# Performance work log

Measured on AMD Instinct MI355X. Metric: run time of the kernel, lower is better.

## Reference

```python
import jax, jax.numpy as jnp
import numpy as np

CAPACITY = 1_000_000
IN_FEATURES = 64
OUT_FEATURES = 64


def setup_inputs() -> dict:
    key = jax.random.key(0)
    k1, k2, k3 = jax.random.split(key, 3)
    query = jax.random.normal(k1, (IN_FEATURES,), dtype=jnp.float32)
    keys = jax.random.normal(k2, (CAPACITY, IN_FEATURES), dtype=jnp.float32)
    values = jax.random.normal(k3, (CAPACITY, OUT_FEATURES), dtype=jnp.float32)
    return {"query": query, "keys": keys, "values": values}


def reference(query, keys, values):
    # attention: [capacity] = keys [C, Din] @ query [Din]
    scores = keys @ query
    attention = jax.nn.softmax(scores, axis=0)
    # out: [Dout] = attention [C] @ values [C, Dout]
    out = attention @ values
    # usage-tracking argmax (softmax is monotone, argmax of scores == argmax of attention)
    amax = jnp.argmax(scores)
    return out, amax
```

## Files before the change

kernel.cpp:

```cpp
#include <hip/hip_runtime.h>
#include <math.h>

#define C_CAP 1000000
#define DIM 64

#define SCORES_OFF 0
#define P1_OFF     1000000
#define HDR_OFF    1010000
#define ACC_OFF    1010064

#define NB1 1024
#define NW1 (NB1 * 4)
#define NTILES (C_CAP / 16)
#define NB3 2048
#define NW3 (NB3 * 4)
#define NCHUNKS (C_CAP / 64)

__global__ __launch_bounds__(256, 4) void nd_scores(
    const float* __restrict__ query,
    const float* __restrict__ keys,
    float* __restrict__ ws, int ntiles, int stride)
{
    const int tid  = threadIdx.x;
    const int lane = tid & 63;
    const int wave = tid >> 6;
    const int cl   = lane & 15;
    const int g    = lane >> 4;
    const int wglobal = blockIdx.x * 4 + wave;

    const float4 q4 = ((const float4*)query)[cl];
    const float4* __restrict__ k4p = (const float4*)keys;

    float m = -1e30f, l = 0.f;

    float4 A0, A1, A2, A3;
    float4 B0, B1, B2, B3;

#define LOADK(b0, b1, b2, b3, tt) {                                        \
        const float4* __restrict__ kp = k4p + (size_t)(tt) * 256 + lane;   \
        b0 = kp[0]; b1 = kp[64]; b2 = kp[128]; b3 = kp[192];               \
    }

#define COMPUTE(b0, b1, b2, b3, tt) {                                          \
        float s0 = fmaf(b0.x, q4.x, fmaf(b0.y, q4.y, fmaf(b0.z, q4.z, b0.w * q4.w))); \
        float s1 = fmaf(b1.x, q4.x, fmaf(b1.y, q4.y, fmaf(b1.z, q4.z, b1.w * q4.w))); \
        float s2 = fmaf(b2.x, q4.x, fmaf(b2.y, q4.y, fmaf(b2.z, q4.z, b2.w * q4.w))); \
        float s3 = fmaf(b3.x, q4.x, fmaf(b3.y, q4.y, fmaf(b3.z, q4.z, b3.w * q4.w))); \
        s0 += __shfl_xor(s0, 1); s1 += __shfl_xor(s1, 1);                      \
        s2 += __shfl_xor(s2, 1); s3 += __shfl_xor(s3, 1);                      \
        s0 += __shfl_xor(s0, 2); s1 += __shfl_xor(s1, 2);                      \
        s2 += __shfl_xor(s2, 2); s3 += __shfl_xor(s3, 2);                      \
        s0 += __shfl_xor(s0, 4); s1 += __shfl_xor(s1, 4);                      \
        s2 += __shfl_xor(s2, 4); s3 += __shfl_xor(s3, 4);                      \
        s0 += __shfl_xor(s0, 8); s1 += __shfl_xor(s1, 8);                      \
        s2 += __shfl_xor(s2, 8); s3 += __shfl_xor(s3, 8);                      \
        const float sv = (cl == 0) ? s0 : (cl == 1) ? s1 : (cl == 2) ? s2 : s3; \
        if (cl < 4) ws[SCORES_OFF + (tt) * 16 + 4 * cl + g] = sv;              \
        l += (__expf(s0) + __expf(s1)) + (__expf(s2) + __expf(s3));            \
        m = fmaxf(m, fmaxf(fmaxf(s0, s1), fmaxf(s2, s3)));                     \
    }

    int t = wglobal;
    LOADK(A0, A1, A2, A3, t);
    while (true) {
        const int tn = t + stride;
        if (tn < ntiles) LOADK(B0, B1, B2, B3, tn);
        COMPUTE(A0, A1, A2, A3, t);
        if (tn >= ntiles) break;
        t = tn + stride;
        if (t < ntiles) LOADK(A0, A1, A2, A3, t);
        COMPUTE(B0, B1, B2, B3, tn);
        if (t >= ntiles) break;
    }

#undef LOADK
#undef COMPUTE

    l += __shfl_xor(l, 16); m = fmaxf(m, __shfl_xor(m, 16));
    l += __shfl_xor(l, 32); m = fmaxf(m, __shfl_xor(m, 32));

    __shared__ float s_m[4], s_l[4];
    if (lane == 0) { s_m[wave] = m; s_l[wave] = l; }
    __syncthreads();
    if (tid == 0) {
        float bm = s_m[0], bl = s_l[0];
        #pragma unroll
        for (int wv = 1; wv < 4; ++wv) {
            bl += s_l[wv];
            bm = fmaxf(bm, s_m[wv]);
        }
        float* bp = ws + P1_OFF + (size_t)blockIdx.x * 4;
        bp[0] = bm;
        bp[1] = bl;
    }
}

__global__ __launch_bounds__(256) void nd_reduce(float* __restrict__ ws, int nb)
{
    const int tid = threadIdx.x;
    float m = -1e30f, l = 0.f;
    for (int b = tid; b < nb; b += 256) {
        const float* bp = ws + P1_OFF + (size_t)b * 4;
        l += bp[1];
        m = fmaxf(m, bp[0]);
    }
    __shared__ float sm[256], sl[256];
    sm[tid] = m; sl[tid] = l;
    __syncthreads();
    for (int s = 128; s > 0; s >>= 1) {
        if (tid < s) {
            sl[tid] += sl[tid + s];
            sm[tid] = fmaxf(sm[tid], sm[tid + s]);
        }
        __syncthreads();
    }
    if (tid == 0) {
        const float M = sm[0];
        ws[HDR_OFF + 0] = M;
        ws[HDR_OFF + 1] = sl[0] * __expf(-M);
        ((int*)ws)[HDR_OFF + 2] = 0;
    }
    if (tid < 64) ws[ACC_OFF + tid] = 0.f;
}

__global__ __launch_bounds__(256, 8) void nd_pv(
    const float* __restrict__ values,
    float* __restrict__ ws, int nchunks, int nwaves_total)
{
    const int tid  = threadIdx.x;
    const int lane = tid & 63;
    const int wave = tid >> 6;
    const int wglobal = blockIdx.x * 4 + wave;

    const float M   = ws[HDR_OFF];
    const float thr = M - 23.0f;
    float acc = 0.f;

    for (int c = wglobal; c < nchunks; c += nwaves_total) {
        const float s = ws[SCORES_OFF + (size_t)c * 64 + lane];
        unsigned long long mask = __ballot(s > thr);
        if (mask) {
            if (s == M) ((int*)ws)[HDR_OFF + 2] = c * 64 + lane;
            const float w = __expf(s - M);
            while (mask) {
                const int b = __ffsll((long long)mask) - 1;
                mask &= mask - 1;
                const float wb = __shfl(w, b);
                acc = fmaf(wb, values[(size_t)(c * 64 + b) * 64 + lane], acc);
            }
        }
    }

    __shared__ float sA[4][64];
    sA[wave][lane] = acc;
    __syncthreads();
    if (tid < 64) {
        const float v = sA[0][tid] + sA[1][tid] + sA[2][tid] + sA[3][tid];
        if (v != 0.f) atomicAdd(ws + ACC_OFF + tid, v);
    }
}

__global__ __launch_bounds__(128) void nd_final(
    const float* __restrict__ ws, float* __restrict__ out)
{
    const int tid = threadIdx.x;
    if (tid < 64) out[tid] = ws[ACC_OFF + tid] / ws[HDR_OFF + 1];
    if (tid == 64) out[64] = (float)((const int*)ws)[HDR_OFF + 2];
}

extern "C" void kernel_launch(void* const* d_in, const int* in_sizes, int n_in,
                              void* d_out, int out_size, void* d_ws, size_t ws_size,
                              hipStream_t stream) {
    const float* query  = (const float*)d_in[0];
    const float* keys   = (const float*)d_in[1];
    const float* values = (const float*)d_in[2];
    float* out = (float*)d_out;
    float* ws  = (float*)d_ws;

    nd_scores<<<NB1, 256, 0, stream>>>(query, keys, ws, NTILES, NW1);
    nd_reduce<<<1, 256, 0, stream>>>(ws, NB1);
    nd_pv<<<NB3, 256, 0, stream>>>(values, ws, NCHUNKS, NW3);
    nd_final<<<1, 128, 0, stream>>>(ws, out);
}
```

Measured before the change: 481.3 us.

## Fuse four launches into one cooperative kernel with grid syncs

Merges the score, reduce, weighted-sum and final kernels into a single cooperative kernel that uses grid.sync between phases. Every block now recomputes the global max and sum redundantly instead of having a separate reduce launch, and the output atomics are replaced by per-block partials reduced in a final phase. This removes launch gaps and the atomics. In exchange it adds grid-wide barrier cost and fixes the PV phase at 1024 blocks instead of 2048, which may lower occupancy for the sparse value gather. The argmax index is no longer reset to zero, so it relies on the max score always being found.

Result: slower. 679.1 us (+41.1%).

```diff
diff --git a/kernel.cpp b/kernel.cpp
--- a/kernel.cpp
+++ b/kernel.cpp
@@ -1,26 +1,31 @@
 #include <hip/hip_runtime.h>
+#include <hip/hip_cooperative_groups.h>
 #include <math.h>
+
+namespace cg = cooperative_groups;
 
 #define C_CAP 1000000
 #define DIM 64
 
+#define NB 1024
+#define NWAVES (NB * 4)
+#define NTILES (C_CAP / 16)
+#define NCHUNKS (C_CAP / 64)
+
 #define SCORES_OFF 0
 #define P1_OFF     1000000
-#define HDR_OFF    1010000
-#define ACC_OFF    1010064
+#define HDR_OFF    1002048
+#define PART_OFF   1002112
 
-#define NB1 1024
-#define NW1 (NB1 * 4)
-#define NTILES (C_CAP / 16)
-#define NB3 2048
-#define NW3 (NB3 * 4)
-#define NCHUNKS (C_CAP / 64)
-
-__global__ __launch_bounds__(256, 4) void nd_scores(
+__global__ __launch_bounds__(256, 4) void nd_fused(
     const float* __restrict__ query,
     const float* __restrict__ keys,
-    float* __restrict__ ws, int ntiles, int stride)
+    const float* __restrict__ values,
+    float* __restrict__ ws,
+    float* __restrict__ out)
 {
+    cg::grid_group grid = cg::this_grid();
+
     const int tid  = threadIdx.x;
     const int lane = tid & 63;
     const int wave = tid >> 6;
@@ -28,13 +33,17 @@
     const int g    = lane >> 4;
     const int wglobal = blockIdx.x * 4 + wave;
 
-    const float4 q4 = ((const float4*)query)[cl];
-    const float4* __restrict__ k4p = (const float4*)keys;
+    __shared__ float s_m4[4], s_l4[4];
+    __shared__ float sm[256], sl[256];
+    __shared__ float sA[4][64];
 
-    float m = -1e30f, l = 0.f;
+    {
+        const float4 q4 = ((const float4*)query)[cl];
+        const float4* __restrict__ k4p = (const float4*)keys;
 
-    float4 A0, A1, A2, A3;
-    float4 B0, B1, B2, B3;
+        float m = -1e30f, l = 0.f;
+        float4 A0, A1, A2, A3;
+        float4 B0, B1, B2, B3;
 
 #define LOADK(b0, b1, b2, b3, tt) {                                        \
         const float4* __restrict__ kp = k4p + (size_t)(tt) * 256 + lane;   \
@@ -60,112 +69,106 @@
         m = fmaxf(m, fmaxf(fmaxf(s0, s1), fmaxf(s2, s3)));                     \
     }
 
-    int t = wglobal;
-    LOADK(A0, A1, A2, A3, t);
-    while (true) {
-        const int tn = t + stride;
-        if (tn < ntiles) LOADK(B0, B1, B2, B3, tn);
-        COMPUTE(A0, A1, A2, A3, t);
-        if (tn >= ntiles) break;
-        t = tn + stride;
-        if (t < ntiles) LOADK(A0, A1, A2, A3, t);
-        COMPUTE(B0, B1, B2, B3, tn);
-        if (t >= ntiles) break;
-    }
-
+        int t = wglobal;
+        LOADK(A0, A1, A2, A3, t);
+        while (true) {
+            const int tn = t + NWAVES;
+            if (tn < NTILES) LOADK(B0, B1, B2, B3, tn);
+            COMPUTE(A0, A1, A2, A3, t);
+            if (tn >= NTILES) break;
+            t = tn + NWAVES;
+            if (t < NTILES) LOADK(A0, A1, A2, A3, t);
+            COMPUTE(B0, B1, B2, B3, tn);
+            if (t >= NTILES) break;
+        }
 #undef LOADK
 #undef COMPUTE
 
-    l += __shfl_xor(l, 16); m = fmaxf(m, __shfl_xor(m, 16));
-    l += __shfl_xor(l, 32); m = fmaxf(m, __shfl_xor(m, 32));
+        l += __shfl_xor(l, 16); m = fmaxf(m, __shfl_xor(m, 16));
+        l += __shfl_xor(l, 32); m = fmaxf(m, __shfl_xor(m, 32));
 
-    __shared__ float s_m[4], s_l[4];
-    if (lane == 0) { s_m[wave] = m; s_l[wave] = l; }
-    __syncthreads();
-    if (tid == 0) {
-        float bm = s_m[0], bl = s_l[0];
-        #pragma unroll
-        for (int wv = 1; wv < 4; ++wv) {
-            bl += s_l[wv];
-            bm = fmaxf(bm, s_m[wv]);
-        }
-        float* bp = ws + P1_OFF + (size_t)blockIdx.x * 4;
-        bp[0] = bm;
-        bp[1] = bl;
-    }
-}
-
-__global__ __launch_bounds__(256) void nd_reduce(float* __restrict__ ws, int nb)
-{
-    const int tid = threadIdx.x;
-    float m = -1e30f, l = 0.f;
-    for (int b = tid; b < nb; b += 256) {
-        const float* bp = ws + P1_OFF + (size_t)b * 4;
-        l += bp[1];
-        m = fmaxf(m, bp[0]);
-    }
-    __shared__ float sm[256], sl[256];
-    sm[tid] = m; sl[tid] = l;
-    __syncthreads();
-    for (int s = 128; s > 0; s >>= 1) {
-        if (tid < s) {
-            sl[tid] += sl[tid + s];
-            sm[tid] = fmaxf(sm[tid], sm[tid + s]);
-        }
+        if (lane == 0) { s_m4[wave] = m; s_l4[wave] = l; }
         __syncthreads();
-    }
-    if (tid == 0) {
-        const float M = sm[0];
-        ws[HDR_OFF + 0] = M;
-        ws[HDR_OFF + 1] = sl[0] * __expf(-M);
-        ((int*)ws)[HDR_OFF + 2] = 0;
-    }
-    if (tid < 64) ws[ACC_OFF + tid] = 0.f;
-}
-
-__global__ __launch_bounds__(256, 8) void nd_pv(
-    const float* __restrict__ values,
-    float* __restrict__ ws, int nchunks, int nwaves_total)
-{
-    const int tid  = threadIdx.x;
-    const int lane = tid & 63;
-    const int wave = tid >> 6;
-    const int wglobal = blockIdx.x * 4 + wave;
-
-    const float M   = ws[HDR_OFF];
-    const float thr = M - 23.0f;
-    float acc = 0.f;
-
-    for (int c = wglobal; c < nchunks; c += nwaves_total) {
-        const float s = ws[SCORES_OFF + (size_t)c * 64 + lane];
-        unsigned long long mask = __ballot(s > thr);
-        if (mask) {
-            if (s == M) ((int*)ws)[HDR_OFF + 2] = c * 64 + lane;
-            const float w = __expf(s - M);
-            while (mask) {
-                const int b = __ffsll((long long)mask) - 1;
-                mask &= mask - 1;
-                const float wb = __shfl(w, b);
-                acc = fmaf(wb, values[(size_t)(c * 64 + b) * 64 + lane], acc);
+        if (tid == 0) {
+            float bm = s_m4[0], bl = s_l4[0];
+            #pragma unroll
+            for (int wv = 1; wv < 4; ++wv) {
+                bl += s_l4[wv];
+                bm = fmaxf(bm, s_m4[wv]);
             }
+            float* bp = ws + P1_OFF + (size_t)blockIdx.x * 2;
+            bp[0] = bm;
+            bp[1] = bl;
         }
     }
 
-    __shared__ float sA[4][64];
-    sA[wave][lane] = acc;
-    __syncthreads();
-    if (tid < 64) {
-        const float v = sA[0][tid] + sA[1][tid] + sA[2][tid] + sA[3][tid];
-        if (v != 0.f) atomicAdd(ws + ACC_OFF + tid, v);
+    grid.sync();
+
+    float M, Ls;
+    {
+        float m = -1e30f, l = 0.f;
+        for (int b = tid; b < NB; b += 256) {
+            const float* bp = ws + P1_OFF + (size_t)b * 2;
+            l += bp[1];
+            m = fmaxf(m, bp[0]);
+        }
+        sm[tid] = m; sl[tid] = l;
+        __syncthreads();
+        for (int s = 128; s > 0; s >>= 1) {
+            if (tid < s) {
+                sl[tid] += sl[tid + s];
+                sm[tid] = fmaxf(sm[tid], sm[tid + s]);
+            }
+            __syncthreads();
+        }
+        M  = sm[0];
+        Ls = sl[0] * __expf(-M);
+        __syncthreads();
     }
-}
 
-__global__ __launch_bounds__(128) void nd_final(
-    const float* __restrict__ ws, float* __restrict__ out)
-{
-    const int tid = threadIdx.x;
-    if (tid < 64) out[tid] = ws[ACC_OFF + tid] / ws[HDR_OFF + 1];
-    if (tid == 64) out[64] = (float)((const int*)ws)[HDR_OFF + 2];
+    {
+        const float thr = M - 23.0f;
+        float acc = 0.f;
+        for (int c = wglobal; c < NCHUNKS; c += NWAVES) {
+            const float s = ws[SCORES_OFF + (size_t)c * 64 + lane];
+            unsigned long long mask = __ballot(s > thr);
+            if (mask) {
+                if (s == M) ((int*)ws)[HDR_OFF] = c * 64 + lane;
+                const float w = __expf(s - M);
+                while (mask) {
+                    const int b = __ffsll((long long)mask) - 1;
+                    mask &= mask - 1;
+                    const float wb = __shfl(w, b);
+                    acc = fmaf(wb, values[(size_t)(c * 64 + b) * 64 + lane], acc);
+                }
+            }
+        }
+        sA[wave][lane] = acc;
+        __syncthreads();
+        if (tid < 64) {
+            ws[PART_OFF + (size_t)blockIdx.x * 64 + tid] =
+                (sA[0][tid] + sA[1][tid]) + (sA[2][tid] + sA[3][tid]);
+        }
+    }
+
+    grid.sync();
+
+    if (blockIdx.x < 64) {
+        const int j = blockIdx.x;
+        float v = 0.f;
+        for (int b = tid; b < NB; b += 256)
+            v += ws[PART_OFF + (size_t)b * 64 + j];
+        sm[tid] = v;
+        __syncthreads();
+        for (int s = 128; s > 0; s >>= 1) {
+            if (tid < s) sm[tid] += sm[tid + s];
+            __syncthreads();
+        }
+        if (tid == 0) {
+            out[j] = sm[0] / Ls;
+            if (j == 0) out[64] = (float)((const int*)ws)[HDR_OFF];
+        }
+    }
 }
 
 extern "C" void kernel_launch(void* const* d_in, const int* in_sizes, int n_in,
@@ -177,8 +180,8 @@
     float* out = (float*)d_out;
     float* ws  = (float*)d_ws;
 
-    nd_scores<<<NB1, 256, 0, stream>>>(query, keys, ws, NTILES, NW1);
-    nd_reduce<<<1, 256, 0, stream>>>(ws, NB1);
-    nd_pv<<<NB3, 256, 0, stream>>>(values, ws, NCHUNKS, NW3);
-    nd_final<<<1, 128, 0, stream>>>(ws, out);
+    void* args[] = { (void*)&query, (void*)&keys, (void*)&values,
+                     (void*)&ws, (void*)&out };
+    hipLaunchCooperativeKernel((void*)nd_fused, dim3(NB), dim3(256),
+                               args, 0, stream);
 }
```

## Compute one key row per lane with scalar-broadcast query

Applied to the files above, without the earlier changes.

Reworks the scores kernel so each lane reads a whole 64-float key row and computes its dot product serially against a query held in uniform registers. This removes the 16-lane shuffle-reduction tree and the conditional scattered score stores, and gives one coalesced score write per lane. The cost is strided per-lane memory access, where each lane reads a 256-byte row at a time, and removal of the explicit double-buffered prefetch. Both could hurt coalescing and latency hiding on a bandwidth-bound stream.

Result: no change. 486.0 us (+1.0%).

```diff
diff --git a/kernel.cpp b/kernel.cpp
--- a/kernel.cpp
+++ b/kernel.cpp
@@ -11,7 +11,7 @@
 
 #define NB1 1024
 #define NW1 (NB1 * 4)
-#define NTILES (C_CAP / 16)
+#define NT64 (C_CAP / 64)
 #define NB3 2048
 #define NW3 (NB3 * 4)
 #define NCHUNKS (C_CAP / 64)
@@ -24,60 +24,40 @@
     const int tid  = threadIdx.x;
     const int lane = tid & 63;
     const int wave = tid >> 6;
-    const int cl   = lane & 15;
-    const int g    = lane >> 4;
     const int wglobal = blockIdx.x * 4 + wave;
 
-    const float4 q4 = ((const float4*)query)[cl];
-    const float4* __restrict__ k4p = (const float4*)keys;
+    float qs[64];
+    #pragma unroll
+    for (int j = 0; j < 64; ++j)
+        qs[j] = __uint_as_float(__builtin_amdgcn_readfirstlane(__float_as_uint(query[j])));
 
     float m = -1e30f, l = 0.f;
 
-    float4 A0, A1, A2, A3;
-    float4 B0, B1, B2, B3;
+    for (int t = wglobal; t < ntiles; t += stride) {
+        const float4* __restrict__ kp =
+            (const float4*)(keys + ((size_t)t * 64 + lane) * 64);
 
-#define LOADK(b0, b1, b2, b3, tt) {                                        \
-        const float4* __restrict__ kp = k4p + (size_t)(tt) * 256 + lane;   \
-        b0 = kp[0]; b1 = kp[64]; b2 = kp[128]; b3 = kp[192];               \
+        float a0 = 0.f, a1 = 0.f, a2 = 0.f, a3 = 0.f;
+        #pragma unroll
+        for (int j = 0; j < 16; ++j) {
+            const float4 k = kp[j];
+            a0 = fmaf(k.x, qs[4 * j + 0], a0);
+            a1 = fmaf(k.y, qs[4 * j + 1], a1);
+            a2 = fmaf(k.z, qs[4 * j + 2], a2);
+            a3 = fmaf(k.w, qs[4 * j + 3], a3);
+        }
+        const float s = (a0 + a1) + (a2 + a3);
+
+        ws[SCORES_OFF + t * 64 + lane] = s;
+        l += __expf(s);
+        m = fmaxf(m, s);
     }
 
-#define COMPUTE(b0, b1, b2, b3, tt) {                                          \
-        float s0 = fmaf(b0.x, q4.x, fmaf(b0.y, q4.y, fmaf(b0.z, q4.z, b0.w * q4.w))); \
-        float s1 = fmaf(b1.x, q4.x, fmaf(b1.y, q4.y, fmaf(b1.z, q4.z, b1.w * q4.w))); \
-        float s2 = fmaf(b2.x, q4.x, fmaf(b2.y, q4.y, fmaf(b2.z, q4.z, b2.w * q4.w))); \
-        float s3 = fmaf(b3.x, q4.x, fmaf(b3.y, q4.y, fmaf(b3.z, q4.z, b3.w * q4.w))); \
-        s0 += __shfl_xor(s0, 1); s1 += __shfl_xor(s1, 1);                      \
-        s2 += __shfl_xor(s2, 1); s3 += __shfl_xor(s3, 1);                      \
-        s0 += __shfl_xor(s0, 2); s1 += __shfl_xor(s1, 2);                      \
-        s2 += __shfl_xor(s2, 2); s3 += __shfl_xor(s3, 2);                      \
-        s0 += __shfl_xor(s0, 4); s1 += __shfl_xor(s1, 4);                      \
-        s2 += __shfl_xor(s2, 4); s3 += __shfl_xor(s3, 4);                      \
-        s0 += __shfl_xor(s0, 8); s1 += __shfl_xor(s1, 8);                      \
-        s2 += __shfl_xor(s2, 8); s3 += __shfl_xor(s3, 8);                      \
-        const float sv = (cl == 0) ? s0 : (cl == 1) ? s1 : (cl == 2) ? s2 : s3; \
-        if (cl < 4) ws[SCORES_OFF + (tt) * 16 + 4 * cl + g] = sv;              \
-        l += (__expf(s0) + __expf(s1)) + (__expf(s2) + __expf(s3));            \
-        m = fmaxf(m, fmaxf(fmaxf(s0, s1), fmaxf(s2, s3)));                     \
+    #pragma unroll
+    for (int off = 1; off <= 32; off <<= 1) {
+        l += __shfl_xor(l, off);
+        m = fmaxf(m, __shfl_xor(m, off));
     }
-
-    int t = wglobal;
-    LOADK(A0, A1, A2, A3, t);
-    while (true) {
-        const int tn = t + stride;
-        if (tn < ntiles) LOADK(B0, B1, B2, B3, tn);
-        COMPUTE(A0, A1, A2, A3, t);
-        if (tn >= ntiles) break;
-        t = tn + stride;
-        if (t < ntiles) LOADK(A0, A1, A2, A3, t);
-        COMPUTE(B0, B1, B2, B3, tn);
-        if (t >= ntiles) break;
-    }
-
-#undef LOADK
-#undef COMPUTE
-
-    l += __shfl_xor(l, 16); m = fmaxf(m, __shfl_xor(m, 16));
-    l += __shfl_xor(l, 32); m = fmaxf(m, __shfl_xor(m, 32));
 
     __shared__ float s_m[4], s_l[4];
     if (lane == 0) { s_m[wave] = m; s_l[wave] = l; }
@@ -177,7 +157,7 @@
     float* out = (float*)d_out;
     float* ws  = (float*)d_ws;
 
-    nd_scores<<<NB1, 256, 0, stream>>>(query, keys, ws, NTILES, NW1);
+    nd_scores<<<NB1, 256, 0, stream>>>(query, keys, ws, NT64, NW1);
     nd_reduce<<<1, 256, 0, stream>>>(ws, NB1);
     nd_pv<<<NB3, 256, 0, stream>>>(values, ws, NCHUNKS, NW3);
     nd_final<<<1, 128, 0, stream>>>(ws, out);
```
